# Kernel optimization log

Hardware: AMD Instinct MI355X
Metric: run time of the kernel (lower is better)

## Reference

```python
import jax, jax.numpy as jnp
import numpy as np

EMBED_DIM = 256
NUM_HEADS = 8
HEAD_DIM = 32
INNER = NUM_HEADS * HEAD_DIM
NEG_SLOPE = 0.2


def setup_inputs() -> dict:
    key = jax.random.key(0)
    ks = jax.random.split(key, 8)
    B, Ns, Nt = 8, 1024, 1024
    src = jax.random.normal(ks[0], (B, Ns, EMBED_DIM), dtype=jnp.float32)
    trg = jax.random.normal(ks[1], (B, Nt, EMBED_DIM), dtype=jnp.float32)
    src_mask = jnp.ones((B, Ns), dtype=bool)
    trg_mask = jax.random.randint(ks[2], (B, Nt), 0, 2).astype(bool)
    # learned params (xavier-ish scale)
    def xavier(k, shape):
        fan_in, fan_out = shape[0], shape[-1]
        lim = (6.0 / (fan_in + fan_out)) ** 0.5
        return jax.random.uniform(k, shape, jnp.float32, -lim, lim)
    W_src = xavier(ks[3], (EMBED_DIM, INNER))
    W_trg = xavier(ks[4], (EMBED_DIM, INNER))  # is_cross_type=True -> independent
    a_src = xavier(ks[5], (NUM_HEADS, HEAD_DIM))
    a_trg = xavier(ks[6], (NUM_HEADS, HEAD_DIM))
    W_out = xavier(ks[7], (INNER, EMBED_DIM))
    return {"src": src, "trg": trg, "src_mask": src_mask, "trg_mask": trg_mask,
            "W_src": W_src, "W_trg": W_trg, "a_src": a_src, "a_trg": a_trg, "W_out": W_out}


def reference(src, trg, src_mask, trg_mask, W_src, W_trg, a_src, a_trg, W_out):
    B, Ns, _ = src.shape
    Nt = trg.shape[1]
    NH, Dh = NUM_HEADS, HEAD_DIM
    src_proj = (src @ W_src).reshape(B, Ns, NH, Dh)  # dropout p=0
    trg_proj = (trg @ W_trg).reshape(B, Nt, NH, Dh)
    score_src = jnp.einsum('bshd,hd->bsh', src_proj, a_src)
    score_trg = jnp.einsum('bthd,hd->bth', trg_proj, a_trg)
    # (B,Ns,NH,1) + (B,1,NH,Nt) -> (B,Ns,NH,Nt)
    scores = score_src[:, :, :, None] + jnp.transpose(score_trg, (0, 2, 1))[:, None, :, :]
    scores = jnp.where(scores >= 0, scores, NEG_SLOPE * scores)  # LeakyReLU
    edge_mask = src_mask[:, :, None, None] & trg_mask[:, None, None, :]
    scores = jnp.where(edge_mask, scores, -jnp.inf)
    attn = jax.nn.softmax(scores, axis=-1)
    attn = jnp.nan_to_num(attn, nan=0.0)
    aggregated = jnp.einsum('bsht,bthd->bshd', attn, trg_proj)
    output = aggregated.reshape(B, Ns, NH * Dh) @ W_out
    return output, jnp.transpose(attn, (0, 2, 1, 3))
```

## Files before the change

### kernel.cpp

```cpp
#include <hip/hip_runtime.h>
#include <hip/hip_bf16.h>
#include <math.h>

#define NB 8
#define NS 1024
#define NT 1024
#define NE 256
#define NHEADS 8
#define DH 32

typedef __attribute__((ext_vector_type(8))) short short8;
typedef __attribute__((ext_vector_type(8))) unsigned short ushort8;
typedef __attribute__((ext_vector_type(4))) float f32x4;

#define O_VT    0u
#define O_AGGB  (4u<<20)
#define O_WTT   (8u<<20)
#define O_WTO   ((8u<<20)+131072u)
#define O_CSRC  ((8u<<20)+262144u)
#define O_CTRG  (O_CSRC+8192u)
#define O_SSRC  (O_CTRG+8192u)
#define O_STRG  (O_SSRC+262144u)
#define O_FLAG  (O_STRG+262144u)

__device__ __forceinline__ unsigned short f2bf(float f) {
    __hip_bfloat16 h = __float2bfloat16(f);
    union { __hip_bfloat16 h; unsigned short u; } c; c.h = h;
    return c.u;
}
__device__ __forceinline__ float bf2f(unsigned short u) {
    union { unsigned u; float f; } x; x.u = ((unsigned)u) << 16;
    return x.f;
}

__global__ __launch_bounds__(256) void setup_kernel(
    const unsigned* __restrict__ tmask_dw, const float* __restrict__ Wsrc,
    const float* __restrict__ Wtrg, const float* __restrict__ Wout,
    const float* __restrict__ asrc, const float* __restrict__ atrg,
    float* __restrict__ c_src, float* __restrict__ c_trg,
    unsigned short* __restrict__ Wt_t, unsigned short* __restrict__ Wt_o,
    int* __restrict__ flag) {
    __shared__ __align__(16) char sm[16640];
    const int tid = threadIdx.x;
    const int bid = blockIdx.x;

    if (bid == 0) {
        __shared__ int s_ok;
        if (tid == 0) s_ok = 1;
        __syncthreads();
        for (int i = tid; i < 2048; i += 256)
            if (tmask_dw[i] > 1u) s_ok = 0;
        __syncthreads();
        if (tid == 0) *flag = s_ok;
    } else if (bid <= 2) {
        float* a_sh = (float*)sm;
        const float* W = (bid == 1) ? Wsrc : Wtrg;
        const float* a = (bid == 1) ? asrc : atrg;
        float* c = (bid == 1) ? c_src : c_trg;
        a_sh[tid] = a[tid];
        __syncthreads();
        const int e = tid;
        float ch[8];
#pragma unroll
        for (int h = 0; h < 8; ++h) ch[h] = 0.f;
        for (int i = 0; i < 64; ++i) {
            const float4 wv = *(const float4*)&W[(size_t)e * NE + i * 4];
            const int h = i >> 3, d0 = (i & 7) * 4;
            ch[h] += wv.x * a_sh[h * 32 + d0] + wv.y * a_sh[h * 32 + d0 + 1] +
                     wv.z * a_sh[h * 32 + d0 + 2] + wv.w * a_sh[h * 32 + d0 + 3];
        }
#pragma unroll
        for (int h = 0; h < 8; ++h) c[h * NE + e] = ch[h];
    } else {
        const int q = bid - 3;
        const float* W = (q >> 4) ? Wout : Wtrg;
        unsigned short* Wt = (q >> 4) ? Wt_o : Wt_t;
        const int tl = q & 15;
        const int k0 = (tl >> 2) * 64, n0 = (tl & 3) * 64;
        float* xs = (float*)sm;
#pragma unroll
        for (int it = 0; it < 4; ++it) {
            const int slot = it * 256 + tid;
            const int k = slot >> 4, c4 = slot & 15;
            const float4 v = *(const float4*)&W[(size_t)(k0 + k) * NE + n0 + c4 * 4];
            float* p = &xs[k * 65 + c4 * 4];
            p[0] = v.x; p[1] = v.y; p[2] = v.z; p[3] = v.w;
        }
        __syncthreads();
#pragma unroll
        for (int it = 0; it < 2; ++it) {
            const int slot = it * 256 + tid;
            const int n = slot >> 3, kc = slot & 7;
            ushort8 v;
#pragma unroll
            for (int e = 0; e < 8; ++e)
                v[e] = f2bf(xs[(kc * 8 + e) * 65 + n]);
            *(ushort8*)&Wt[(size_t)(n0 + n) * NE + k0 + kc * 8] = v;
        }
    }
}

__global__ __launch_bounds__(256) void mid_kernel(
    const float* __restrict__ src, const float* __restrict__ trg,
    const float* __restrict__ c_src, const float* __restrict__ c_trg,
    const unsigned short* __restrict__ Wt_t, unsigned short* __restrict__ Vt,
    float* __restrict__ ssrc, float* __restrict__ strg) {
    __shared__ __align__(16) char sm[49152];
    const int tid = threadIdx.x;
    const int bid = blockIdx.x;

    if (bid < 256) {
        unsigned short* As = (unsigned short*)sm;
        unsigned short* ldsT = (unsigned short*)(sm + 32768);
        const int lane = tid & 63, w = tid >> 6;
        const int row0 = (bid >> 1) * 64;
        const int col0 = (bid & 1) * 128;

#pragma unroll
        for (int it = 0; it < 8; ++it) {
            const int gf = it * 256 + tid;
            const int row = gf >> 5, g3 = gf & 31;
            const float4 a = *(const float4*)&trg[(size_t)(row0 + row) * NE + g3 * 8];
            const float4 b = *(const float4*)&trg[(size_t)(row0 + row) * NE + g3 * 8 + 4];
            ushort8 v;
            v[0] = f2bf(a.x); v[1] = f2bf(a.y); v[2] = f2bf(a.z); v[3] = f2bf(a.w);
            v[4] = f2bf(b.x); v[5] = f2bf(b.y); v[6] = f2bf(b.z); v[7] = f2bf(b.w);
            *(ushort8*)&As[row * NE + ((g3 ^ (row & 7)) * 8)] = v;
        }
        __syncthreads();

        const int r = lane & 15, g = lane >> 4;
        short8 af[8];
#pragma unroll
        for (int kk = 0; kk < 8; ++kk)
            af[kk] = *(const short8*)&As[(w * 16 + r) * NE + (((kk * 4 + g) ^ (r & 7)) * 8)];

        f32x4 acc[8];
#pragma unroll
        for (int nt = 0; nt < 8; ++nt) acc[nt] = (f32x4){0.f, 0.f, 0.f, 0.f};
#pragma unroll
        for (int kk = 0; kk < 8; ++kk) {
#pragma unroll
            for (int nt = 0; nt < 8; ++nt) {
                const int col = col0 + nt * 16 + r;
                const short8 bf = *(const short8*)&Wt_t[(size_t)col * NE + kk * 32 + g * 8];
                acc[nt] = __builtin_amdgcn_mfma_f32_16x16x32_bf16(af[kk], bf, acc[nt], 0, 0, 0);
            }
        }
        __syncthreads();

#pragma unroll
        for (int nt = 0; nt < 8; ++nt) {
            const int cl = nt * 16 + r;
            const int sw = (cl & 7) << 3;
#pragma unroll
            for (int j = 0; j < 4; ++j) {
                const int t = w * 16 + g * 4 + j;
                ldsT[cl * 64 + (t ^ sw)] = f2bf(acc[nt][j]);
            }
        }
        __syncthreads();

        const int b = row0 >> 10, t0 = row0 & 1023;
#pragma unroll
        for (int it = 0; it < 4; ++it) {
            const int slot = it * 256 + tid;
            const int cl = slot >> 3, ch = slot & 7;
            const int colg = col0 + cl;
            const int h = colg >> 5, d = colg & 31;
            *(ushort8*)&Vt[(((size_t)(b * 8 + h)) * 32 + d) * 1024 + t0 + ch * 8] =
                *(const ushort8*)&ldsT[cl * 64 + ch * 8];
        }
    } else {
        float* xs = (float*)sm;
        float* cs = (float*)(sm + 32768);
        const int rowg0 = (bid - 256) * 32;
        const bool is_src = rowg0 < NB * NS;
        const float* X = is_src ? (src + (size_t)rowg0 * NE)
                                : (trg + (size_t)(rowg0 - NB * NS) * NE);
        const float* C = is_src ? c_src : c_trg;
        float* S = is_src ? (ssrc + (size_t)rowg0 * NHEADS)
                          : (strg + (size_t)(rowg0 - NB * NS) * NHEADS);

#pragma unroll
        for (int it = 0; it < 8; ++it) {
            const int slot = it * 256 + tid;
            const int row = slot >> 6, c4 = slot & 63;
            *(float4*)&xs[row * NE + c4 * 4] =
                *(const float4*)&X[(size_t)row * NE + c4 * 4];
            cs[slot] = C[slot];
        }
        __syncthreads();

        const int r = tid >> 3, h = tid & 7;
        float s = 0.f;
        for (int e = 0; e < NE; e += 4) {
            const float4 x = *(const float4*)&xs[r * NE + e];
            const float4 c = *(const float4*)&cs[h * NE + e];
            s += x.x * c.x + x.y * c.y + x.z * c.z + x.w * c.w;
        }
        S[(size_t)r * NHEADS + h] = s;
    }
}

__global__ __launch_bounds__(256) void fused_softmax_agg_kernel(
    const float* __restrict__ ssrc, const float* __restrict__ strg,
    const void* __restrict__ smask, const void* __restrict__ tmask,
    const int* __restrict__ flag_p, const unsigned short* __restrict__ Vt,
    float* __restrict__ attn, unsigned short* __restrict__ agg_bf) {
    const int blk = blockIdx.x;
    const int stile = blk & 15;
    const int h = (blk >> 4) & 7;
    const int b = blk >> 7;
    const int tid = threadIdx.x;
    const int lane = tid & 63;
    const int wave = tid >> 6;
    const int flag = *flag_p;

    __shared__ __align__(16) float s_sm[NT];
    __shared__ __align__(16) unsigned short vt[32 * 1024];
    __shared__ float s_inv[64];

    const unsigned short* vsrc = Vt + (size_t)(b * NHEADS + h) * 32768;
#pragma unroll
    for (int it = 0; it < 16; ++it) {
        const int off = (it * 256 + tid) * 8;
        *(ushort8*)&vt[off] = *(const ushort8*)&vsrc[off];
    }
    for (int t = tid; t < NT; t += 256) {
        const bool mv = flag ? (((const int*)tmask)[b * NT + t] != 0)
                             : (((const unsigned char*)tmask)[b * NT + t] != 0);
        s_sm[t] = mv ? strg[((size_t)b * NT + t) * NHEADS + h] : -1e30f;
    }
    __syncthreads();

    const int r = lane & 15;
    const int g = lane >> 4;
    const int srow = stile * 64 + wave * 16 + r;
    const float ss = ssrc[((size_t)b * NS + srow) * NHEADS + h];
    const bool rowv = flag ? (((const int*)smask)[b * NS + srow] != 0)
                           : (((const unsigned char*)smask)[b * NS + srow] != 0);
    const int sw = (r & 7) << 3;
    const unsigned short* vr0 = vt + r * 1024;
    const unsigned short* vr1 = vt + (r + 16) * 1024;

    short8 preg[32];
    f32x4 acc0 = {0.f, 0.f, 0.f, 0.f};
    f32x4 acc1 = {0.f, 0.f, 0.f, 0.f};
    float sum = 0.f;

#pragma unroll
    for (int c = 0; c < 32; ++c) {
        const int tb = c * 32 + g * 8;
        const float4 v0 = *(const float4*)&s_sm[tb];
        const float4 v1 = *(const float4*)&s_sm[tb + 4];
        const float vv[8] = {v0.x, v0.y, v0.z, v0.w, v1.x, v1.y, v1.z, v1.w};
        short8 pa;
#pragma unroll
        for (int e = 0; e < 8; ++e) {
            float v = ss + vv[e];
            v = (v >= 0.f) ? v : 0.2f * v;
            const float p = __expf(v);
            sum += p;
            pa[e] = (short)f2bf(p);
        }
        preg[c] = pa;
        const short8 b0 = *(const short8*)&vr0[tb ^ sw];
        const short8 b1 = *(const short8*)&vr1[tb ^ sw];
        acc0 = __builtin_amdgcn_mfma_f32_16x16x32_bf16(pa, b0, acc0, 0, 0, 0);
        acc1 = __builtin_amdgcn_mfma_f32_16x16x32_bf16(pa, b1, acc1, 0, 0, 0);
    }

    sum += __shfl_xor(sum, 16);
    sum += __shfl_xor(sum, 32);
    const float inv = (rowv && sum > 0.f) ? 1.f / sum : 0.f;
    if (g == 0) s_inv[wave * 16 + r] = inv;

    float* arow = attn + ((size_t)((b * NHEADS + h) * NS) + srow) * NT;
#pragma unroll
    for (int c = 0; c < 32; ++c) {
        const int tb = c * 32 + g * 8;
        float o[8];
#pragma unroll
        for (int e = 0; e < 8; ++e)
            o[e] = bf2f((unsigned short)preg[c][e]) * inv;
        const float4 o0 = {o[0], o[1], o[2], o[3]};
        const float4 o1 = {o[4], o[5], o[6], o[7]};
        *(float4*)(arow + tb) = o0;
        *(float4*)(arow + tb + 4) = o1;
    }

    __syncthreads();
    const int orow = stile * 64 + wave * 16 + g * 4;
    unsigned short* ab = agg_bf + ((size_t)b * NS + orow) * NE + h * DH + r;
#pragma unroll
    for (int j = 0; j < 4; ++j) {
        const float iv = s_inv[wave * 16 + g * 4 + j];
        ab[(size_t)j * NE] = f2bf(acc0[j] * iv);
        ab[(size_t)j * NE + 16] = f2bf(acc1[j] * iv);
    }
}

__global__ __launch_bounds__(256) void gemm_out_kernel(
    const unsigned short* __restrict__ Xb, const unsigned short* __restrict__ Wt,
    float* __restrict__ Yf) {
    __shared__ __align__(16) unsigned short As[64 * NE];
    const int tid = threadIdx.x;
    const int lane = tid & 63;
    const int w = tid >> 6;
    const int row0 = blockIdx.x * 64;
    const int col0 = blockIdx.y * 128;

#pragma unroll
    for (int it = 0; it < 8; ++it) {
        const int gf = it * 256 + tid;
        const int row = gf >> 5, g3 = gf & 31;
        const ushort8 v = *(const ushort8*)&Xb[(size_t)(row0 + row) * NE + g3 * 8];
        *(ushort8*)&As[row * NE + ((g3 ^ (row & 7)) * 8)] = v;
    }
    __syncthreads();

    const int r = lane & 15, g = lane >> 4;
    short8 af[8];
#pragma unroll
    for (int kk = 0; kk < 8; ++kk)
        af[kk] = *(const short8*)&As[(w * 16 + r) * NE + (((kk * 4 + g) ^ (r & 7)) * 8)];

    f32x4 acc[8];
#pragma unroll
    for (int nt = 0; nt < 8; ++nt) acc[nt] = (f32x4){0.f, 0.f, 0.f, 0.f};
#pragma unroll
    for (int kk = 0; kk < 8; ++kk) {
#pragma unroll
        for (int nt = 0; nt < 8; ++nt) {
            const int col = col0 + nt * 16 + r;
            const short8 bf = *(const short8*)&Wt[(size_t)col * NE + kk * 32 + g * 8];
            acc[nt] = __builtin_amdgcn_mfma_f32_16x16x32_bf16(af[kk], bf, acc[nt], 0, 0, 0);
        }
    }

#pragma unroll
    for (int nt = 0; nt < 8; ++nt) {
        const int col = col0 + nt * 16 + r;
#pragma unroll
        for (int j = 0; j < 4; ++j) {
            const int row = row0 + w * 16 + g * 4 + j;
            Yf[(size_t)row * NE + col] = acc[nt][j];
        }
    }
}

extern "C" void kernel_launch(void* const* d_in, const int* in_sizes, int n_in,
                              void* d_out, int out_size, void* d_ws, size_t ws_size,
                              hipStream_t stream) {
    const float* src   = (const float*)d_in[0];
    const float* trg   = (const float*)d_in[1];
    const void*  smask = d_in[2];
    const void*  tmask = d_in[3];
    const float* Wsrc  = (const float*)d_in[4];
    const float* Wtrg  = (const float*)d_in[5];
    const float* asrc  = (const float*)d_in[6];
    const float* atrg  = (const float*)d_in[7];
    const float* Wout  = (const float*)d_in[8];

    float* out  = (float*)d_out;
    float* attn = out + (size_t)NB * NS * NE;

    char* wsb = (char*)d_ws;
    unsigned short* Vt     = (unsigned short*)(wsb + O_VT);
    unsigned short* agg_bf = (unsigned short*)(wsb + O_AGGB);
    unsigned short* Wt_t   = (unsigned short*)(wsb + O_WTT);
    unsigned short* Wt_o   = (unsigned short*)(wsb + O_WTO);
    float* c_src = (float*)(wsb + O_CSRC);
    float* c_trg = (float*)(wsb + O_CTRG);
    float* ssrc  = (float*)(wsb + O_SSRC);
    float* strg  = (float*)(wsb + O_STRG);
    int*   flag  = (int*)(wsb + O_FLAG);

    setup_kernel<<<35, 256, 0, stream>>>(
        (const unsigned*)tmask, Wsrc, Wtrg, Wout, asrc, atrg,
        c_src, c_trg, Wt_t, Wt_o, flag);

    mid_kernel<<<768, 256, 0, stream>>>(
        src, trg, c_src, c_trg, Wt_t, Vt, ssrc, strg);

    fused_softmax_agg_kernel<<<NB * NHEADS * (NS / 64), 256, 0, stream>>>(
        ssrc, strg, smask, tmask, flag, Vt, attn, agg_bf);

    gemm_out_kernel<<<dim3(128, 2), 256, 0, stream>>>(agg_bf, Wt_o, out);
}
```

Measured before the change: 112.3 us.

## Recompute softmax exponentials in two passes and read V directly from global memory

```diff
diff --git a/kernel.cpp b/kernel.cpp
--- a/kernel.cpp
+++ b/kernel.cpp
@@ -218,15 +218,8 @@
     const int flag = *flag_p;
 
     __shared__ __align__(16) float s_sm[NT];
-    __shared__ __align__(16) unsigned short vt[32 * 1024];
     __shared__ float s_inv[64];
 
-    const unsigned short* vsrc = Vt + (size_t)(b * NHEADS + h) * 32768;
-#pragma unroll
-    for (int it = 0; it < 16; ++it) {
-        const int off = (it * 256 + tid) * 8;
-        *(ushort8*)&vt[off] = *(const ushort8*)&vsrc[off];
-    }
     for (int t = tid; t < NT; t += 256) {
         const bool mv = flag ? (((const int*)tmask)[b * NT + t] != 0)
                              : (((const unsigned char*)tmask)[b * NT + t] != 0);
@@ -241,53 +234,55 @@
     const bool rowv = flag ? (((const int*)smask)[b * NS + srow] != 0)
                            : (((const unsigned char*)smask)[b * NS + srow] != 0);
     const int sw = (r & 7) << 3;
-    const unsigned short* vr0 = vt + r * 1024;
-    const unsigned short* vr1 = vt + (r + 16) * 1024;
-
-    short8 preg[32];
-    f32x4 acc0 = {0.f, 0.f, 0.f, 0.f};
-    f32x4 acc1 = {0.f, 0.f, 0.f, 0.f};
+    const unsigned short* vr0 = Vt + (size_t)(b * NHEADS + h) * 32768 + r * 1024;
+    const unsigned short* vr1 = vr0 + 16 * 1024;
+
     float sum = 0.f;
-
-#pragma unroll
+#pragma unroll 4
     for (int c = 0; c < 32; ++c) {
         const int tb = c * 32 + g * 8;
         const float4 v0 = *(const float4*)&s_sm[tb];
         const float4 v1 = *(const float4*)&s_sm[tb + 4];
         const float vv[8] = {v0.x, v0.y, v0.z, v0.w, v1.x, v1.y, v1.z, v1.w};
-        short8 pa;
 #pragma unroll
         for (int e = 0; e < 8; ++e) {
             float v = ss + vv[e];
             v = (v >= 0.f) ? v : 0.2f * v;
-            const float p = __expf(v);
-            sum += p;
-            pa[e] = (short)f2bf(p);
-        }
-        preg[c] = pa;
-        const short8 b0 = *(const short8*)&vr0[tb ^ sw];
-        const short8 b1 = *(const short8*)&vr1[tb ^ sw];
-        acc0 = __builtin_amdgcn_mfma_f32_16x16x32_bf16(pa, b0, acc0, 0, 0, 0);
-        acc1 = __builtin_amdgcn_mfma_f32_16x16x32_bf16(pa, b1, acc1, 0, 0, 0);
-    }
-
+            sum += __expf(v);
+        }
+    }
     sum += __shfl_xor(sum, 16);
     sum += __shfl_xor(sum, 32);
     const float inv = (rowv && sum > 0.f) ? 1.f / sum : 0.f;
     if (g == 0) s_inv[wave * 16 + r] = inv;
 
+    f32x4 acc0 = {0.f, 0.f, 0.f, 0.f};
+    f32x4 acc1 = {0.f, 0.f, 0.f, 0.f};
     float* arow = attn + ((size_t)((b * NHEADS + h) * NS) + srow) * NT;
-#pragma unroll
+
+#pragma unroll 4
     for (int c = 0; c < 32; ++c) {
         const int tb = c * 32 + g * 8;
-        float o[8];
-#pragma unroll
-        for (int e = 0; e < 8; ++e)
-            o[e] = bf2f((unsigned short)preg[c][e]) * inv;
-        const float4 o0 = {o[0], o[1], o[2], o[3]};
-        const float4 o1 = {o[4], o[5], o[6], o[7]};
+        const short8 b0 = *(const short8*)&vr0[tb ^ sw];
+        const short8 b1 = *(const short8*)&vr1[tb ^ sw];
+        const float4 v0 = *(const float4*)&s_sm[tb];
+        const float4 v1 = *(const float4*)&s_sm[tb + 4];
+        const float vv[8] = {v0.x, v0.y, v0.z, v0.w, v1.x, v1.y, v1.z, v1.w};
+        float p[8];
+        short8 pa;
+#pragma unroll
+        for (int e = 0; e < 8; ++e) {
+            float v = ss + vv[e];
+            v = (v >= 0.f) ? v : 0.2f * v;
+            p[e] = __expf(v);
+            pa[e] = (short)f2bf(p[e]);
+        }
+        const float4 o0 = {p[0] * inv, p[1] * inv, p[2] * inv, p[3] * inv};
+        const float4 o1 = {p[4] * inv, p[5] * inv, p[6] * inv, p[7] * inv};
         *(float4*)(arow + tb) = o0;
         *(float4*)(arow + tb + 4) = o1;
+        acc0 = __builtin_amdgcn_mfma_f32_16x16x32_bf16(pa, b0, acc0, 0, 0, 0);
+        acc1 = __builtin_amdgcn_mfma_f32_16x16x32_bf16(pa, b1, acc1, 0, 0, 0);
     }
 
     __syncthreads();
```

New measurement: 104.4 us. 7.0% less time.
